# Optimization experiments

Hardware: AMD Instinct MI355X
Metric: run time of the kernel (lower is better)

The kernel has to match this reference:

```python
import jax, jax.numpy as jnp
import numpy as np


def setup_inputs() -> dict:
    key = jax.random.key(0)
    k1, k2 = jax.random.split(key)
    inputs = jax.random.normal(k1, (2, 1600, 1600, 3), dtype=jnp.float32)
    # matches TruncatedNormal(stddev=20) scale of the learned offsets
    delta_p = 20.0 * jax.random.normal(k2, (2, 4, 4, 2), dtype=jnp.float32)
    return {"inputs": inputs, "delta_p": delta_p, "k": 4, "crop_size": 384}


def reference(inputs, delta_p, k, crop_size):
    # Faithful, gather-based version of the original dense bilinear-kernel sum:
    # G((x,y),(px,py)) = max(0,1-|x-px|)*max(0,1-|y-py|) summed over the whole
    # image == standard bilinear interpolation with zero padding outside.
    B, H, W, C = inputs.shape
    cs = crop_size
    pl = (H - cs * k) // 2
    pr = (W - cs * k) // 2
    s = jnp.arange(cs, dtype=jnp.float32)
    bi = jnp.arange(k, dtype=jnp.float32)
    # rows[t,i,j,s] = pl + i*cs + s + delta_p[t,i,j,0]
    rows = pl + bi[None, :, None, None] * cs + s[None, None, None, :] + delta_p[..., 0][..., None]
    # cols[t,i,j,s] = pr + j*cs + s + delta_p[t,i,j,1]
    cols = pr + bi[None, None, :, None] * cs + s[None, None, None, :] + delta_p[..., 1][..., None]
    rows = rows.reshape(B, -1)  # (B, k*k*cs), bin order i-major/j-minor as in the loop
    cols = cols.reshape(B, -1)

    def sample(img, r, c):
        # img (H,W,C); r,c (N,) fractional coords. 4-corner bilinear gather.
        r0 = jnp.floor(r)
        c0 = jnp.floor(c)
        rf = r - r0
        cf = c - c0
        out = jnp.zeros(r.shape + (img.shape[-1],), img.dtype)
        for dr, wr in ((0.0, 1.0 - rf), (1.0, rf)):
            ri = r0 + dr
            rvalid = (ri >= 0) & (ri < img.shape[0])
            rii = jnp.clip(ri, 0, img.shape[0] - 1).astype(jnp.int32)
            for dc, wc in ((0.0, 1.0 - cf), (1.0, cf)):
                ci = c0 + dc
                valid = rvalid & (ci >= 0) & (ci < img.shape[1])
                cii = jnp.clip(ci, 0, img.shape[1] - 1).astype(jnp.int32)
                w = jnp.where(valid, wr * wc, 0.0)
                out = out + w[:, None] * img[rii, cii]
        return out

    v = jax.vmap(sample)(inputs, rows, cols)  # (B, k*k*cs, C)
    # The original builds p with np.tile for BOTH axes, so every output row r
    # within a bin samples the same cs points -> rows are identical copies.
    v = v.reshape(B, k * k, 1, cs, C)
    return jnp.broadcast_to(v, (B, k * k, cs, cs, C))
```

## Files before the change

kernel.cpp:

```cpp
#include <hip/hip_runtime.h>


constexpr int B  = 2;
constexpr int H  = 1600;
constexpr int W  = 1600;
constexpr int C  = 3;
constexpr int K  = 4;
constexpr int CS = 384;
constexpr int PL = (H - CS * K) / 2;
constexpr int ROW_F  = CS * C;
constexpr int ROW_F4 = ROW_F / 4;
constexpr int NBBIN  = B * K * K;
constexpr int RCHUNK = 8;
constexpr int NCHUNK = CS / RCHUNK;
constexpr int K2_ITERS = RCHUNK * ROW_F4 / 256;

__global__ __launch_bounds__(128) void roideform_gather(
    const float* __restrict__ img,
    const float* __restrict__ dp,
    float* __restrict__ ws)
{
    const int bbin = blockIdx.x / 3;
    const int s    = (blockIdx.x % 3) * 128 + threadIdx.x;
    const int b    = bbin >> 4;
    const int bin  = bbin & 15;
    const int i    = bin >> 2;
    const int j    = bin & 3;

    const float dp0 = dp[((b * K + i) * K + j) * 2 + 0];
    const float dp1 = dp[((b * K + i) * K + j) * 2 + 1];
    const float* __restrict__ imgb = img + (size_t)b * H * W * C;

    const float r = (float)(PL + i * CS + s) + dp0;
    const float c = (float)(PL + j * CS + s) + dp1;
    const float r0 = floorf(r), c0 = floorf(c);
    const float rf = r - r0,   cf = c - c0;
    const int ri0 = (int)r0, ci0 = (int)c0;

    float acc0 = 0.f, acc1 = 0.f, acc2 = 0.f;
#pragma unroll
    for (int dr = 0; dr < 2; ++dr) {
        const int  ri = ri0 + dr;
        const float wr = dr ? rf : (1.0f - rf);
        const bool rvalid = (ri >= 0) && (ri < H);
#pragma unroll
        for (int dc = 0; dc < 2; ++dc) {
            const int  ci = ci0 + dc;
            const float wc = dc ? cf : (1.0f - cf);
            if (rvalid && (ci >= 0) && (ci < W)) {
                const float w = wr * wc;
                const float* p = imgb + ((size_t)ri * W + ci) * C;
                acc0 += w * p[0];
                acc1 += w * p[1];
                acc2 += w * p[2];
            }
        }
    }
    float* o = ws + ((size_t)bbin * CS + s) * C;
    o[0] = acc0;
    o[1] = acc1;
    o[2] = acc2;
}

__global__ __launch_bounds__(256) void roideform_bcast(
    const float* __restrict__ ws,
    float* __restrict__ out)
{
    const int bid   = blockIdx.x;
    const int bbin  = bid / NCHUNK;
    const int chunk = bid - bbin * NCHUNK;

    __shared__ float4 row[ROW_F4];
    const float4* __restrict__ ws4 = (const float4*)ws + (size_t)bbin * ROW_F4;
    for (int t = threadIdx.x; t < ROW_F4; t += 256) row[t] = ws4[t];
    __syncthreads();

    float4* __restrict__ out4 =
        (float4*)out + (size_t)(bbin * CS + chunk * RCHUNK) * ROW_F4;

#pragma unroll
    for (int it = 0; it < K2_ITERS; ++it) {
        const int t = it * 256 + (int)threadIdx.x;
        out4[t] = row[t % ROW_F4];
    }
}

extern "C" void kernel_launch(void* const* d_in, const int* in_sizes, int n_in,
                              void* d_out, int out_size, void* d_ws, size_t ws_size,
                              hipStream_t stream) {
    const float* img = (const float*)d_in[0];
    const float* dp  = (const float*)d_in[1];
    float* out = (float*)d_out;
    float* ws  = (float*)d_ws;

    roideform_gather<<<NBBIN * 3, 128, 0, stream>>>(img, dp, ws);
    roideform_bcast<<<NBBIN * NCHUNK, 256, 0, stream>>>(ws, out);
}
```

Measured before the change: 108.0 us.

## Fuse gather and broadcast kernels, recompute row per block, nontemporal stores

Merges the bilinear gather kernel and the broadcast kernel into one launch. Each broadcast block now recomputes its bin's 384-sample row straight into shared memory instead of reading it from a workspace, which removes one launch and the workspace round-trip. The output stores become nontemporal so the write-only output does not pollute the cache. The cost is that the gather is redundantly recomputed by each of the 48 chunk blocks per bin, adding extra image reads.

```diff
diff --git a/kernel.cpp b/kernel.cpp
--- a/kernel.cpp
+++ b/kernel.cpp
@@ -1,5 +1,7 @@
 #include <hip/hip_runtime.h>
 
+
+typedef float f32x4 __attribute__((ext_vector_type(4)));
 
 constexpr int B  = 2;
 constexpr int H  = 1600;
@@ -13,75 +15,67 @@
 constexpr int NBBIN  = B * K * K;
 constexpr int RCHUNK = 8;
 constexpr int NCHUNK = CS / RCHUNK;
-constexpr int K2_ITERS = RCHUNK * ROW_F4 / 256;
+constexpr int NSTORE = RCHUNK * ROW_F4 / 256;
 
-__global__ __launch_bounds__(128) void roideform_gather(
+__global__ __launch_bounds__(256) void roideform_fused(
     const float* __restrict__ img,
     const float* __restrict__ dp,
-    float* __restrict__ ws)
+    float* __restrict__ out)
 {
-    const int bbin = blockIdx.x / 3;
-    const int s    = (blockIdx.x % 3) * 128 + threadIdx.x;
+    const int bid   = blockIdx.x;
+    const int bbin  = bid / NCHUNK;
+    const int chunk = bid - bbin * NCHUNK;
     const int b    = bbin >> 4;
     const int bin  = bbin & 15;
     const int i    = bin >> 2;
     const int j    = bin & 3;
 
+    __shared__ f32x4 row4s[ROW_F4];
+    float* row = (float*)row4s;
+
     const float dp0 = dp[((b * K + i) * K + j) * 2 + 0];
     const float dp1 = dp[((b * K + i) * K + j) * 2 + 1];
     const float* __restrict__ imgb = img + (size_t)b * H * W * C;
 
-    const float r = (float)(PL + i * CS + s) + dp0;
-    const float c = (float)(PL + j * CS + s) + dp1;
-    const float r0 = floorf(r), c0 = floorf(c);
-    const float rf = r - r0,   cf = c - c0;
-    const int ri0 = (int)r0, ci0 = (int)c0;
+    for (int s = (int)threadIdx.x; s < CS; s += 256) {
+        const float r = (float)(PL + i * CS + s) + dp0;
+        const float c = (float)(PL + j * CS + s) + dp1;
+        const float r0 = floorf(r), c0 = floorf(c);
+        const float rf = r - r0,   cf = c - c0;
+        const int ri0 = (int)r0, ci0 = (int)c0;
 
-    float acc0 = 0.f, acc1 = 0.f, acc2 = 0.f;
+        float a0 = 0.f, a1 = 0.f, a2 = 0.f;
 #pragma unroll
-    for (int dr = 0; dr < 2; ++dr) {
-        const int  ri = ri0 + dr;
-        const float wr = dr ? rf : (1.0f - rf);
-        const bool rvalid = (ri >= 0) && (ri < H);
+        for (int dr = 0; dr < 2; ++dr) {
+            const int  ri = ri0 + dr;
+            const float wr = dr ? rf : (1.0f - rf);
+            const bool rvalid = (ri >= 0) && (ri < H);
 #pragma unroll
-        for (int dc = 0; dc < 2; ++dc) {
-            const int  ci = ci0 + dc;
-            const float wc = dc ? cf : (1.0f - cf);
-            if (rvalid && (ci >= 0) && (ci < W)) {
-                const float w = wr * wc;
-                const float* p = imgb + ((size_t)ri * W + ci) * C;
-                acc0 += w * p[0];
-                acc1 += w * p[1];
-                acc2 += w * p[2];
+            for (int dc = 0; dc < 2; ++dc) {
+                const int  ci = ci0 + dc;
+                const float wc = dc ? cf : (1.0f - cf);
+                if (rvalid && (ci >= 0) && (ci < W)) {
+                    const float w = wr * wc;
+                    const float* p = imgb + ((size_t)ri * W + ci) * C;
+                    a0 += w * p[0];
+                    a1 += w * p[1];
+                    a2 += w * p[2];
+                }
             }
         }
+        row[s * C + 0] = a0;
+        row[s * C + 1] = a1;
+        row[s * C + 2] = a2;
     }
-    float* o = ws + ((size_t)bbin * CS + s) * C;
-    o[0] = acc0;
-    o[1] = acc1;
-    o[2] = acc2;
-}
-
-__global__ __launch_bounds__(256) void roideform_bcast(
-    const float* __restrict__ ws,
-    float* __restrict__ out)
-{
-    const int bid   = blockIdx.x;
-    const int bbin  = bid / NCHUNK;
-    const int chunk = bid - bbin * NCHUNK;
-
-    __shared__ float4 row[ROW_F4];
-    const float4* __restrict__ ws4 = (const float4*)ws + (size_t)bbin * ROW_F4;
-    for (int t = threadIdx.x; t < ROW_F4; t += 256) row[t] = ws4[t];
     __syncthreads();
 
-    float4* __restrict__ out4 =
-        (float4*)out + (size_t)(bbin * CS + chunk * RCHUNK) * ROW_F4;
+    f32x4* __restrict__ out4 =
+        (f32x4*)out + (size_t)(bbin * CS + chunk * RCHUNK) * ROW_F4;
 
 #pragma unroll
-    for (int it = 0; it < K2_ITERS; ++it) {
+    for (int it = 0; it < NSTORE; ++it) {
         const int t = it * 256 + (int)threadIdx.x;
-        out4[t] = row[t % ROW_F4];
+        __builtin_nontemporal_store(row4s[t % ROW_F4], out4 + t);
     }
 }
 
@@ -91,8 +85,7 @@
     const float* img = (const float*)d_in[0];
     const float* dp  = (const float*)d_in[1];
     float* out = (float*)d_out;
-    float* ws  = (float*)d_ws;
+    (void)d_ws; (void)ws_size;
 
-    roideform_gather<<<NBBIN * 3, 128, 0, stream>>>(img, dp, ws);
-    roideform_bcast<<<NBBIN * NCHUNK, 256, 0, stream>>>(ws, out);
+    roideform_fused<<<NBBIN * NCHUNK, 256, 0, stream>>>(img, dp, out);
 }
```

Result: slower. 114.5 us (+6.0%).
